# Kernel tuning notes

Hardware: AMD Instinct MI355X
Metric: run time of the kernel (lower is better)

Reference implementation:

```python
import jax, jax.numpy as jnp
import numpy as np

EMBED_DIM = 768
N_HEADS = 12
HEAD_SIZE = EMBED_DIM // N_HEADS


def setup_inputs() -> dict:
    key = jax.random.key(0)
    k1, k2, k3, k4 = jax.random.split(key, 4)
    B, T, C = 512, 128, EMBED_DIM
    x = jax.random.normal(k1, (B, T, C), dtype=jnp.float32)
    # torch Linear weights: [out, in]
    w_qkv = jax.random.normal(k2, (3 * C, C), dtype=jnp.float32) / np.sqrt(C)
    w_proj = jax.random.normal(k3, (C, C), dtype=jnp.float32) / np.sqrt(C)
    b_proj = jax.random.normal(k4, (C,), dtype=jnp.float32) * 0.01
    return {"x": x, "w_qkv": w_qkv, "w_proj": w_proj, "b_proj": b_proj}


def reference(x, w_qkv, w_proj, b_proj):
    B, T, C = x.shape
    H, D = N_HEADS, HEAD_SIZE
    qkv = jnp.einsum('btc,oc->bto', x, w_qkv)  # [B,T,3C]
    q, k, v = jnp.split(qkv, 3, axis=-1)
    # [B,T,C] -> [B,H,T,D]
    q = q.reshape(B, T, H, D).transpose(0, 2, 1, 3)
    k = k.reshape(B, T, H, D).transpose(0, 2, 1, 3)
    v = v.reshape(B, T, H, D).transpose(0, 2, 1, 3)
    wei = jnp.einsum('bhtd,bhsd->bhts', q, k)  # [B,H,T,T]
    causal = jnp.tril(jnp.ones((T, T), dtype=bool))  # True where allowed
    wei = jnp.where(causal, wei, -jnp.inf)
    # original scales AFTER masking (-inf stays -inf)
    wei = jax.nn.softmax(wei / jnp.sqrt(jnp.asarray(D, x.dtype)), axis=-1)
    out = jnp.einsum('bhts,bhsd->bhtd', wei, v)  # [B,H,T,D]
    out = out.transpose(0, 2, 1, 3).reshape(B, T, C)
    # proj; dropout is identity in eval mode
    out = jnp.einsum('btc,oc->bto', out, w_proj) + b_proj
    return out
```

## Files before the change

kernel.cpp:

```cpp
#include <hip/hip_runtime.h>
#include <hip/hip_bf16.h>

typedef __bf16 bf16_t;
typedef __attribute__((ext_vector_type(8))) __bf16 bf16x8;
typedef __attribute__((ext_vector_type(4))) float f32x4;

#define B_SZ 512
#define T_SZ 128
#define C_SZ 768
#define H_SZ 12
#define D_SZ 64
#define M_SZ (B_SZ * T_SZ)
#define NQKV (3 * C_SZ)

__global__ __launch_bounds__(256) void cvt_f32_bf16(
    const float* __restrict__ in, bf16_t* __restrict__ out, int n)
{
    int i = (blockIdx.x * blockDim.x + threadIdx.x) * 8;
    int stride = gridDim.x * blockDim.x * 8;
    for (; i < n; i += stride) {
        float4 a = *reinterpret_cast<const float4*>(in + i);
        float4 b = *reinterpret_cast<const float4*>(in + i + 4);
        bf16x8 o;
        o[0] = (bf16_t)a.x; o[1] = (bf16_t)a.y;
        o[2] = (bf16_t)a.z; o[3] = (bf16_t)a.w;
        o[4] = (bf16_t)b.x; o[5] = (bf16_t)b.y;
        o[6] = (bf16_t)b.z; o[7] = (bf16_t)b.w;
        *reinterpret_cast<bf16x8*>(out + i) = o;
    }
}

__device__ __forceinline__ void gload16(const bf16_t* g, const char* l)
{
    __builtin_amdgcn_global_load_lds(
        (const __attribute__((address_space(1))) void*)g,
        (__attribute__((address_space(3))) void*)l, 16, 0, 0);
}

#define BAR() do { asm volatile("" ::: "memory"); \
                   __builtin_amdgcn_s_barrier(); \
                   asm volatile("" ::: "memory"); } while (0)

#define VMC(n) asm volatile("s_waitcnt vmcnt(" #n ")" ::: "memory")

#define LGKM0() do { asm volatile("s_waitcnt lgkmcnt(0)" ::: "memory"); \
                     __builtin_amdgcn_sched_barrier(0); } while (0)

#define RD_A0(bb) do { _Pragma("unroll") for (int m_ = 0; m_ < 4; ++m_) { \
    af0[m_][0] = *(const bf16x8*)(rdAk0 + (bb)*32768 + m_*2048); \
    af0[m_][1] = *(const bf16x8*)(rdAk1 + (bb)*32768 + m_*2048); } } while (0)

#define RD_AY(bb) do { _Pragma("unroll") for (int m_ = 0; m_ < 4; ++m_) { \
    afY[m_][0] = *(const bf16x8*)(rdAk0 + (bb)*32768 + 8192 + m_*2048); \
    afY[m_][1] = *(const bf16x8*)(rdAk1 + (bb)*32768 + 8192 + m_*2048); } } while (0)

#define RD_B01(bb) do { _Pragma("unroll") for (int n_ = 0; n_ < 2; ++n_) { \
    b01[n_][0] = *(const bf16x8*)(rdBk0 + (bb)*32768 + n_*2048); \
    b01[n_][1] = *(const bf16x8*)(rdBk1 + (bb)*32768 + n_*2048); } } while (0)

#define RD_B23(bb) do { _Pragma("unroll") for (int n_ = 0; n_ < 2; ++n_) { \
    b23[n_][0] = *(const bf16x8*)(rdBk0 + (bb)*32768 + 4096 + n_*2048); \
    b23[n_][1] = *(const bf16x8*)(rdBk1 + (bb)*32768 + 4096 + n_*2048); } } while (0)

#define ST_A(bb, hf, u) do { if ((u) < nt) { \
    const bf16_t* s_ = pA + (size_t)((hf)*128) * K + (size_t)(u)*64; \
    char* d_ = ldsAw + (bb)*32768 + (hf)*16384; \
    gload16(s_, d_); gload16(s_ + (size_t)8*K, d_ + 1024); } } while (0)

#define ST_B(bb, hf, u) do { if ((u) < nt) { \
    const bf16_t* s_ = pB + (size_t)((hf)*128) * K + (size_t)(u)*64; \
    char* d_ = ldsBw + (bb)*32768 + (hf)*16384; \
    gload16(s_, d_); gload16(s_ + (size_t)8*K, d_ + 1024); } } while (0)

#define MFQ(A_, B_, mo, no) do { __builtin_amdgcn_s_setprio(1); \
    _Pragma("unroll") for (int m_ = 0; m_ < 4; ++m_) \
    _Pragma("unroll") for (int n_ = 0; n_ < 2; ++n_) { \
        acc[(mo)+m_][(no)+n_] = __builtin_amdgcn_mfma_f32_16x16x32_bf16( \
            A_[m_][0], B_[n_][0], acc[(mo)+m_][(no)+n_], 0, 0, 0); \
        acc[(mo)+m_][(no)+n_] = __builtin_amdgcn_mfma_f32_16x16x32_bf16( \
            A_[m_][1], B_[n_][1], acc[(mo)+m_][(no)+n_], 0, 0, 0); } \
    __builtin_amdgcn_s_setprio(0); } while (0)

template <bool BF16_OUT, bool BIAS>
__global__ __launch_bounds__(512, 2) void gemm256(
    const bf16_t* __restrict__ A, const bf16_t* __restrict__ Bt,
    void* __restrict__ Cout, const float* __restrict__ bias,
    int M, int N, int K, int nx)
{
    __shared__ char smem[131072];

    const int tid  = threadIdx.x;
    const int lane = tid & 63;
    const int w    = tid >> 6;
    const int wr   = w >> 2;
    const int wc   = w & 3;

    const int nwg = gridDim.x;
    int bid = blockIdx.x;
    if ((nwg & 7) == 0) bid = (bid & 7) * (nwg >> 3) + (bid >> 3);
    const int bx = bid % nx;
    const int by = bid / nx;
    const size_t bm = (size_t)by * 256;
    const size_t bn = (size_t)bx * 256;

    const int nt    = K >> 6;
    const int niter = nt >> 1;

    const int i3    = lane >> 3;
    const int colSw = ((lane & 7) ^ i3) * 8;
    const bf16_t* pA = A  + (bm + (size_t)(w * 16 + i3)) * K + colSw;
    const bf16_t* pB = Bt + (bn + (size_t)(w * 16 + i3)) * K + colSw;
    char* ldsAw = smem + w * 2048;
    char* ldsBw = smem + 65536 + w * 2048;

    const int lane_lo = lane & 15;
    const int sxr  = (lane & 7) << 4;
    const int cK0  = (((lane >> 4) * 16) ^ sxr);
    const int cK1  = cK0 ^ 64;
    const char* rdAk0 = smem + wr * 16384 + lane_lo * 128 + cK0;
    const char* rdAk1 = smem + wr * 16384 + lane_lo * 128 + cK1;
    const char* rdBk0 = smem + 65536 + (wc >> 1) * 16384 + ((wc & 1) * 64 + lane_lo) * 128 + cK0;
    const char* rdBk1 = smem + 65536 + (wc >> 1) * 16384 + ((wc & 1) * 64 + lane_lo) * 128 + cK1;

    f32x4  acc[8][4] = {};
    bf16x8 af0[4][2], afY[4][2], b01[2][2], b23[2][2];

    ST_B(0, 0, 0); ST_A(0, 0, 0); ST_A(0, 1, 0); ST_B(0, 1, 0);
    ST_B(1, 0, 1); ST_A(1, 0, 1);
    VMC(4);
    BAR();

    for (int it = 0; it < niter; ++it) {
        const int u = it * 2;
        const bool last = (it + 1 == niter);
        RD_A0(0); RD_B01(0); RD_B23(0); ST_A(1, 1, u + 1); MFQ(af0, b01, 0, 0); BAR();
        RD_AY(0);                        ST_B(1, 1, u + 1); MFQ(af0, b23, 0, 2); BAR();
                                         ST_B(0, 0, u + 2); MFQ(afY, b01, 4, 0); BAR();
                                         ST_A(0, 0, u + 2); MFQ(afY, b23, 4, 2);
        if (last) { VMC(0); } else { VMC(4); }
        BAR();
        RD_A0(1); RD_B01(1); RD_B23(1); ST_A(0, 1, u + 2); MFQ(af0, b01, 0, 0); BAR();
        RD_AY(1);                        ST_B(0, 1, u + 2); MFQ(af0, b23, 0, 2); BAR();
                                         ST_B(1, 0, u + 3); MFQ(afY, b01, 4, 0); BAR();
                                         ST_A(1, 0, u + 3); MFQ(afY, b23, 4, 2);
        if (last) { VMC(0); } else { VMC(4); }
        BAR();
    }

    const int crow = (lane >> 4) * 4;
    const int ccol = lane & 15;
    if constexpr (BF16_OUT) {
        char* ep = smem + w * 16384;
        #pragma unroll
        for (int n = 0; n < 4; ++n) {
            const size_t col = bn + wc * 64 + n * 16 + ccol;
            float bv = 0.f;
            if constexpr (BIAS) bv = bias[col];
            #pragma unroll
            for (int m = 0; m < 8; ++m)
                #pragma unroll
                for (int r = 0; r < 4; ++r)
                    *(bf16_t*)(ep + (m * 16 + crow + r) * 128 + (n * 16 + ccol) * 2)
                        = (bf16_t)(acc[m][n][r] + bv);
        }
        LGKM0();
        bf16_t* cb = (bf16_t*)Cout;
        #pragma unroll
        for (int pass = 0; pass < 16; ++pass) {
            const int rloc = pass * 8 + (lane >> 3);
            const int ch   = lane & 7;
            bf16x8 v = *(const bf16x8*)(ep + rloc * 128 + ch * 16);
            *(bf16x8*)((char*)(cb + (bm + wr * 128 + rloc) * (size_t)N + bn + wc * 64) + ch * 16) = v;
        }
    } else {
        #pragma unroll
        for (int n = 0; n < 4; ++n) {
            const size_t col = bn + wc * 64 + n * 16 + ccol;
            float bv = 0.f;
            if constexpr (BIAS) bv = bias[col];
            #pragma unroll
            for (int m = 0; m < 8; ++m) {
                #pragma unroll
                for (int r = 0; r < 4; ++r) {
                    const size_t row = bm + wr * 128 + m * 16 + crow + r;
                    ((float*)Cout)[row * N + col] = acc[m][n][r] + bv;
                }
            }
        }
    }
}

__global__ __launch_bounds__(256) void attn_kernel(
    const bf16_t* __restrict__ qkv, bf16_t* __restrict__ outp)
{
    __shared__ bf16_t Ks[128 * 64];
    __shared__ bf16_t Vt[64 * 128];
    __shared__ bf16_t Ps[128 * 128];

    const int h    = blockIdx.x;
    const int b    = blockIdx.y;
    const int tid  = threadIdx.x;
    const int lane = tid & 63;
    const int wave = tid >> 6;

    const bf16_t* base = qkv + (size_t)b * T_SZ * NQKV + h * D_SZ;

    #pragma unroll
    for (int p = 0; p < 4; ++p) {
        int e   = p * 256 + tid;
        int row = e >> 3;
        int col = (e & 7) * 8;
        int4 kv = *reinterpret_cast<const int4*>(base + (size_t)row * NQKV + C_SZ + col);
        int kb = row * 128 + ((col * 2) ^ ((row & 7) << 4));
        *reinterpret_cast<int4*>((char*)Ks + kb) = kv;

        bf16x8 vv = *reinterpret_cast<const bf16x8*>(base + (size_t)row * NQKV + 2 * C_SZ + col);
        #pragma unroll
        for (int j = 0; j < 8; ++j) {
            int d  = col + j;
            int vb = d * 256 + ((row * 2) ^ ((d & 7) << 4));
            *reinterpret_cast<bf16_t*>((char*)Vt + vb) = vv[j];
        }
    }

    bf16x8 qf[2][2];
    #pragma unroll
    for (int mi = 0; mi < 2; ++mi)
        #pragma unroll
        for (int ks = 0; ks < 2; ++ks) {
            int m = wave * 32 + mi * 16 + (lane & 15);
            int d = ks * 32 + (lane >> 4) * 8;
            qf[mi][ks] = *reinterpret_cast<const bf16x8*>(base + (size_t)m * NQKV + d);
        }

    __syncthreads();

    f32x4 s[2][8] = {};
    #pragma unroll
    for (int ks = 0; ks < 2; ++ks) {
        int koff = ks * 32 + (lane >> 4) * 8;
        #pragma unroll
        for (int nj = 0; nj < 8; ++nj) {
            int n  = nj * 16 + (lane & 15);
            int kb = n * 128 + ((koff * 2) ^ ((n & 7) << 4));
            bf16x8 kf = *reinterpret_cast<const bf16x8*>((char*)Ks + kb);
            #pragma unroll
            for (int mi = 0; mi < 2; ++mi)
                s[mi][nj] = __builtin_amdgcn_mfma_f32_16x16x32_bf16(
                    qf[mi][ks], kf, s[mi][nj], 0, 0, 0);
        }
    }

    const float scale = 0.125f;
    #pragma unroll
    for (int mi = 0; mi < 2; ++mi) {
        #pragma unroll
        for (int r = 0; r < 4; ++r) {
            int m = wave * 32 + mi * 16 + ((lane >> 4) << 2) + r;
            float sv[8];
            float mx = -3.0e38f;
            #pragma unroll
            for (int nj = 0; nj < 8; ++nj) {
                int n   = nj * 16 + (lane & 15);
                float v = s[mi][nj][r] * scale;
                v = (n <= m) ? v : -3.0e38f;
                sv[nj] = v;
                mx = fmaxf(mx, v);
            }
            #pragma unroll
            for (int off = 1; off < 16; off <<= 1)
                mx = fmaxf(mx, __shfl_xor(mx, off));
            float sum = 0.f;
            #pragma unroll
            for (int nj = 0; nj < 8; ++nj) {
                float p = __expf(sv[nj] - mx);
                sv[nj] = p;
                sum += p;
            }
            #pragma unroll
            for (int off = 1; off < 16; off <<= 1)
                sum += __shfl_xor(sum, off);
            float inv = 1.0f / sum;
            #pragma unroll
            for (int nj = 0; nj < 8; ++nj) {
                int n  = nj * 16 + (lane & 15);
                int pb = m * 256 + ((n * 2) ^ ((m & 7) << 4));
                *reinterpret_cast<bf16_t*>((char*)Ps + pb) = (bf16_t)(sv[nj] * inv);
            }
        }
    }

    __syncthreads();

    f32x4 o[2][4] = {};
    #pragma unroll
    for (int ks = 0; ks < 4; ++ks) {
        int soff = ks * 32 + (lane >> 4) * 8;
        bf16x8 pf[2];
        #pragma unroll
        for (int mi = 0; mi < 2; ++mi) {
            int m  = wave * 32 + mi * 16 + (lane & 15);
            int pb = m * 256 + ((soff * 2) ^ ((m & 7) << 4));
            pf[mi] = *reinterpret_cast<const bf16x8*>((char*)Ps + pb);
        }
        #pragma unroll
        for (int nj = 0; nj < 4; ++nj) {
            int d  = nj * 16 + (lane & 15);
            int vb = d * 256 + ((soff * 2) ^ ((d & 7) << 4));
            bf16x8 vf = *reinterpret_cast<const bf16x8*>((char*)Vt + vb);
            #pragma unroll
            for (int mi = 0; mi < 2; ++mi)
                o[mi][nj] = __builtin_amdgcn_mfma_f32_16x16x32_bf16(
                    pf[mi], vf, o[mi][nj], 0, 0, 0);
        }
    }

    __syncthreads();

    char* on = (char*)Ps;
    #pragma unroll
    for (int mi = 0; mi < 2; ++mi)
        #pragma unroll
        for (int nj = 0; nj < 4; ++nj)
            #pragma unroll
            for (int r = 0; r < 4; ++r) {
                int m = wave * 32 + mi * 16 + ((lane >> 4) << 2) + r;
                int d = nj * 16 + (lane & 15);
                *(bf16_t*)(on + m * 128 + d * 2) = (bf16_t)o[mi][nj][r];
            }

    __syncthreads();

    bf16_t* op = outp + (size_t)b * T_SZ * C_SZ + h * D_SZ;
    #pragma unroll
    for (int pass = 0; pass < 4; ++pass) {
        int row = pass * 32 + (tid >> 3);
        int ch  = tid & 7;
        bf16x8 v = *(const bf16x8*)(on + row * 128 + ch * 16);
        *(bf16x8*)((char*)(op + (size_t)row * C_SZ) + ch * 16) = v;
    }
}

extern "C" void kernel_launch(void* const* d_in, const int* in_sizes, int n_in,
                              void* d_out, int out_size, void* d_ws, size_t ws_size,
                              hipStream_t stream)
{
    const float* x      = (const float*)d_in[0];
    const float* w_qkv  = (const float*)d_in[1];
    const float* w_proj = (const float*)d_in[2];
    const float* b_proj = (const float*)d_in[3];

    const int n_x     = M_SZ * C_SZ;
    const int n_wqkv  = NQKV * C_SZ;
    const int n_wproj = C_SZ * C_SZ;

    char* ws = (char*)d_ws;
    bf16_t* xb     = (bf16_t*)ws;
    bf16_t* wqkvb  = (bf16_t*)(ws + (size_t)n_x * 2);
    bf16_t* wprojb = (bf16_t*)(ws + (size_t)n_x * 2 + (size_t)n_wqkv * 2);
    bf16_t* qkvb   = (bf16_t*)(ws + (size_t)n_x * 2 + (size_t)n_wqkv * 2 + (size_t)n_wproj * 2);
    bf16_t* attnb  = xb;

    cvt_f32_bf16<<<4096, 256, 0, stream>>>(x, xb, n_x);
    cvt_f32_bf16<<<(n_wqkv / 8 + 255) / 256, 256, 0, stream>>>(w_qkv, wqkvb, n_wqkv);
    cvt_f32_bf16<<<(n_wproj / 8 + 255) / 256, 256, 0, stream>>>(w_proj, wprojb, n_wproj);

    gemm256<true, false><<<dim3((NQKV / 256) * (M_SZ / 256)), 512, 0, stream>>>(
        xb, wqkvb, qkvb, nullptr, M_SZ, NQKV, C_SZ, NQKV / 256);

    attn_kernel<<<dim3(H_SZ, B_SZ), 256, 0, stream>>>(qkvb, attnb);

    gemm256<false, true><<<dim3((C_SZ / 256) * (M_SZ / 256)), 512, 0, stream>>>(
        attnb, wprojb, d_out, b_proj, M_SZ, C_SZ, C_SZ, C_SZ / 256);
}
```

Before: 523.5 us.

## Fuse fp32-to-bf16 conversion of x into the QKV GEMM A-tile loader

Drops the standalone kernel that converts x to bf16. The QKV GEMM now reads fp32 A tiles straight into registers, converts them and writes them to swizzled LDS while the B operand is still loaded asynchronously. This avoids writing and rereading a 100MB bf16 copy of x. In exchange, the A operand is read as fp32 once per N-tile (9 times), which doubles A traffic in the GEMM and raises register pressure.

After: 889.8 us. 70.0% more time.

```diff
diff --git a/kernel.cpp b/kernel.cpp
--- a/kernel.cpp
+++ b/kernel.cpp
@@ -43,6 +43,8 @@
 
 #define VMC(n) asm volatile("s_waitcnt vmcnt(" #n ")" ::: "memory")
 
+#define LGKMW() asm volatile("s_waitcnt lgkmcnt(0)" ::: "memory")
+
 #define LGKM0() do { asm volatile("s_waitcnt lgkmcnt(0)" ::: "memory"); \
                      __builtin_amdgcn_sched_barrier(0); } while (0)
 
@@ -80,6 +82,117 @@
         acc[(mo)+m_][(no)+n_] = __builtin_amdgcn_mfma_f32_16x16x32_bf16( \
             A_[m_][1], B_[n_][1], acc[(mo)+m_][(no)+n_], 0, 0, 0); } \
     __builtin_amdgcn_s_setprio(0); } while (0)
+
+#define ALOAD(u) do { if ((u) < nt) { \
+    const float* s_ = pAf + (size_t)(u) * 64; \
+    _Pragma("unroll") for (int j_ = 0; j_ < 4; ++j_) { \
+        av[j_*2]   = *(const float4*)(s_ + (size_t)(8*j_) * K); \
+        av[j_*2+1] = *(const float4*)(s_ + (size_t)(8*j_) * K + 4); } } } while (0)
+
+#define AWRITE(u, bb) do { if ((u) < nt) { \
+    _Pragma("unroll") for (int j_ = 0; j_ < 4; ++j_) { \
+        bf16x8 o_; \
+        o_[0] = (bf16_t)av[j_*2].x;   o_[1] = (bf16_t)av[j_*2].y; \
+        o_[2] = (bf16_t)av[j_*2].z;   o_[3] = (bf16_t)av[j_*2].w; \
+        o_[4] = (bf16_t)av[j_*2+1].x; o_[5] = (bf16_t)av[j_*2+1].y; \
+        o_[6] = (bf16_t)av[j_*2+1].z; o_[7] = (bf16_t)av[j_*2+1].w; \
+        *(bf16x8*)(ldsAwr + (bb)*32768 + j_*1024) = o_; } } } while (0)
+
+__global__ __launch_bounds__(512, 2) void gemm1_f32a(
+    const float* __restrict__ A, const bf16_t* __restrict__ Bt,
+    bf16_t* __restrict__ Cout, int M, int N, int K, int nx)
+{
+    __shared__ char smem[131072];
+
+    const int tid  = threadIdx.x;
+    const int lane = tid & 63;
+    const int w    = tid >> 6;
+    const int wr   = w >> 2;
+    const int wc   = w & 3;
+
+    const int nwg = gridDim.x;
+    int bid = blockIdx.x;
+    if ((nwg & 7) == 0) bid = (bid & 7) * (nwg >> 3) + (bid >> 3);
+    const int bx = bid % nx;
+    const int by = bid / nx;
+    const size_t bm = (size_t)by * 256;
+    const size_t bn = (size_t)bx * 256;
+
+    const int nt    = K >> 6;
+    const int niter = nt >> 1;
+
+    const int i3    = lane >> 3;
+    const int colSw = ((lane & 7) ^ i3) * 8;
+    const bf16_t* pB = Bt + (bn + (size_t)(w * 16 + i3)) * K + colSw;
+    char* ldsBw = smem + 65536 + w * 2048;
+
+    const int s8 = lane & 7;
+    const int r8 = lane >> 3;
+    const float* pAf = A + (bm + (size_t)(w * 32 + r8)) * K + s8 * 8;
+    char* ldsAwr = smem + (w >> 2) * 16384 + ((w & 3) * 32 + r8) * 128 + ((s8 ^ r8) * 16);
+
+    const int lane_lo = lane & 15;
+    const int sxr  = (lane & 7) << 4;
+    const int cK0  = (((lane >> 4) * 16) ^ sxr);
+    const int cK1  = cK0 ^ 64;
+    const char* rdAk0 = smem + wr * 16384 + lane_lo * 128 + cK0;
+    const char* rdAk1 = smem + wr * 16384 + lane_lo * 128 + cK1;
+    const char* rdBk0 = smem + 65536 + (wc >> 1) * 16384 + ((wc & 1) * 64 + lane_lo) * 128 + cK0;
+    const char* rdBk1 = smem + 65536 + (wc >> 1) * 16384 + ((wc & 1) * 64 + lane_lo) * 128 + cK1;
+
+    f32x4  acc[8][4] = {};
+    bf16x8 af0[4][2], afY[4][2], b01[2][2], b23[2][2];
+    float4 av[8];
+
+    ALOAD(0); AWRITE(0, 0);
+    ST_B(0, 0, 0); ST_B(0, 1, 0);
+    ALOAD(1);
+    VMC(8);
+    LGKMW();
+    BAR();
+
+    for (int it = 0; it < niter; ++it) {
+        const int u = it * 2;
+        const bool lastit = (it + 1 == niter);
+        ST_B(1, 0, u + 1); ST_B(1, 1, u + 1);
+        AWRITE(u + 1, 1);
+        ALOAD(u + 2);
+        RD_A0(0); RD_B01(0); RD_B23(0); RD_AY(0);
+        MFQ(af0, b01, 0, 0); MFQ(af0, b23, 0, 2);
+        MFQ(afY, b01, 4, 0); MFQ(afY, b23, 4, 2);
+        if (lastit) { VMC(0); } else { VMC(8); }
+        LGKMW(); BAR();
+        ST_B(0, 0, u + 2); ST_B(0, 1, u + 2);
+        AWRITE(u + 2, 0);
+        ALOAD(u + 3);
+        RD_A0(1); RD_B01(1); RD_B23(1); RD_AY(1);
+        MFQ(af0, b01, 0, 0); MFQ(af0, b23, 0, 2);
+        MFQ(afY, b01, 4, 0); MFQ(afY, b23, 4, 2);
+        if (lastit) { VMC(0); } else { VMC(8); }
+        LGKMW(); BAR();
+    }
+
+    const int crow = (lane >> 4) * 4;
+    const int ccol = lane & 15;
+    char* ep = smem + w * 16384;
+    #pragma unroll
+    for (int n = 0; n < 4; ++n) {
+        #pragma unroll
+        for (int m = 0; m < 8; ++m)
+            #pragma unroll
+            for (int r = 0; r < 4; ++r)
+                *(bf16_t*)(ep + (m * 16 + crow + r) * 128 + (n * 16 + ccol) * 2)
+                    = (bf16_t)acc[m][n][r];
+    }
+    LGKM0();
+    #pragma unroll
+    for (int pass = 0; pass < 16; ++pass) {
+        const int rloc = pass * 8 + (lane >> 3);
+        const int ch   = lane & 7;
+        bf16x8 v = *(const bf16x8*)(ep + rloc * 128 + ch * 16);
+        *(bf16x8*)((char*)(Cout + (bm + wr * 128 + rloc) * (size_t)N + bn + wc * 64) + ch * 16) = v;
+    }
+}
 
 template <bool BF16_OUT, bool BIAS>
 __global__ __launch_bounds__(512, 2) void gemm256(
@@ -350,23 +463,21 @@
     const float* w_proj = (const float*)d_in[2];
     const float* b_proj = (const float*)d_in[3];
 
-    const int n_x     = M_SZ * C_SZ;
     const int n_wqkv  = NQKV * C_SZ;
     const int n_wproj = C_SZ * C_SZ;
 
     char* ws = (char*)d_ws;
-    bf16_t* xb     = (bf16_t*)ws;
-    bf16_t* wqkvb  = (bf16_t*)(ws + (size_t)n_x * 2);
-    bf16_t* wprojb = (bf16_t*)(ws + (size_t)n_x * 2 + (size_t)n_wqkv * 2);
-    bf16_t* qkvb   = (bf16_t*)(ws + (size_t)n_x * 2 + (size_t)n_wqkv * 2 + (size_t)n_wproj * 2);
-    bf16_t* attnb  = xb;
-
-    cvt_f32_bf16<<<4096, 256, 0, stream>>>(x, xb, n_x);
+    bf16_t* wqkvb  = (bf16_t*)ws;
+    bf16_t* wprojb = (bf16_t*)(ws + (size_t)n_wqkv * 2);
+    bf16_t* qkvb   = (bf16_t*)(ws + (size_t)n_wqkv * 2 + (size_t)n_wproj * 2);
+    bf16_t* attnb  = (bf16_t*)(ws + (size_t)n_wqkv * 2 + (size_t)n_wproj * 2
+                                  + (size_t)M_SZ * NQKV * 2);
+
     cvt_f32_bf16<<<(n_wqkv / 8 + 255) / 256, 256, 0, stream>>>(w_qkv, wqkvb, n_wqkv);
     cvt_f32_bf16<<<(n_wproj / 8 + 255) / 256, 256, 0, stream>>>(w_proj, wprojb, n_wproj);
 
-    gemm256<true, false><<<dim3((NQKV / 256) * (M_SZ / 256)), 512, 0, stream>>>(
-        xb, wqkvb, qkvb, nullptr, M_SZ, NQKV, C_SZ, NQKV / 256);
+    gemm1_f32a<<<dim3((NQKV / 256) * (M_SZ / 256)), 512, 0, stream>>>(
+        x, wqkvb, qkvb, M_SZ, NQKV, C_SZ, NQKV / 256);
 
     attn_kernel<<<dim3(H_SZ, B_SZ), 256, 0, stream>>>(qkvb, attnb);
 
```
